# Performance work log

Measured on AMD Instinct MI355X. Metric: run time of the kernel, lower is better.

Reference implementation:

```python
import jax, jax.numpy as jnp
import numpy as np

TEMPERATURE = 11.313708498984761  # sqrt(128)
TOP_K = 16
EPS = 10e-8


def sparse_attention(attn_s, top_k):
    # attn_s: [N, T]; keep top_k entries per row, shift by k-th value, clamp, renormalize
    T = attn_s.shape[1]
    if T <= top_k:
        return attn_s
    delta = jax.lax.top_k(attn_s, top_k)[0][:, -1] + EPS  # [N]
    w = jnp.maximum(attn_s - delta[:, None], 0.0)
    return w / (jnp.sum(w, axis=1, keepdims=True) + EPS)


def setup_inputs() -> dict:
    key = jax.random.key(0)
    kq, kk, kv = jax.random.split(key, 3)
    q = jax.random.normal(kq, (8, 4096, 128), dtype=jnp.float32)
    k = jax.random.normal(kk, (8, 4096, 128), dtype=jnp.float32)
    v = jax.random.normal(kv, (8, 1, 128), dtype=jnp.float32)
    return {"q": q, "k": k, "v": v}


def reference(q, k, v):
    # scores: [b, lq, lk]
    scores = jnp.einsum('bqd,bkd->bqk', q, k) / TEMPERATURE
    # max over keys (keepdim) then exp -> [b, lq, 1]
    scores = jnp.exp(jnp.max(scores, axis=-1, keepdims=True))
    b, lq, _ = scores.shape
    # flag=True: softmax over the query dimension (permute(0,2,1) then softmax(-1))
    attn = jax.nn.softmax(scores[:, :, 0], axis=-1)  # [b, lq]
    # Sparse_attention top-k over query dim (flag=True reshape path)
    sp = sparse_attention(attn, TOP_K)  # [b, lq]
    attn3 = sp[:, :, None]  # [b, lq, 1] (dropout p=0.0 -> identity)
    out = jnp.einsum('bqk,bkd->bqd', attn3, v)  # [b, lq, dv]
    extra_loss = 0.0
    return out, attn3, extra_loss
```

## Files before the change

### kernel.cpp

```cpp
#include <hip/hip_runtime.h>
#include <math.h>

typedef __attribute__((ext_vector_type(8)))  short short8v;
typedef __attribute__((ext_vector_type(4)))  short short4v;
typedef __attribute__((ext_vector_type(16))) float f32x16;

#define NB     8
#define SEQ    4096
#define DIM    128
#define KSPLIT 4
#define NSPAN  (SEQ / KSPLIT)
#define BN     64
#define BM     256
#define TEMP_INV (1.0f / 11.313708498984761f)
#define EPSF   1e-7f
#define NEGINF -3.0e38f

__device__ __forceinline__ unsigned short f2bf(float x) {
    unsigned u = __float_as_uint(x);
    return (unsigned short)((u + 0x7FFFu + ((u >> 16) & 1u)) >> 16);
}
__device__ __forceinline__ float bf2f(unsigned short h) {
    return __uint_as_float(((unsigned)h) << 16);
}

#define GL_LDS16(gsrc, ldst)                                                              \
    __builtin_amdgcn_global_load_lds((const __attribute__((address_space(1))) void*)(gsrc), \
                                     (__attribute__((address_space(3))) void*)(ldst), 16, 0, 0)

__global__ __launch_bounds__(256) void split_k_kernel(
    const float* __restrict__ kp, unsigned short* __restrict__ ks)
{
    int t    = blockIdx.x * 256 + threadIdx.x;
    int row  = t >> 3;
    int soct = t & 7;
    const float* src = kp + (size_t)row * DIM + soct * 16;
    unsigned short* dst = ks + (size_t)row * 256;
    int key = (row & 15) << 3;
    #pragma unroll
    for (int i = 0; i < 4; ++i) {
        float4 x = *(const float4*)(src + i * 4);
        int p = (soct * 16 + i * 4) ^ key;
        float xs[4] = {x.x, x.y, x.z, x.w};
        short4v h, l;
        #pragma unroll
        for (int j = 0; j < 4; ++j) {
            unsigned short hb = f2bf(xs[j]);
            h[j] = (short)hb;
            l[j] = (short)f2bf(xs[j] - bf2f(hb));
        }
        *(short4v*)(dst + p)       = h;
        *(short4v*)(dst + 128 + p) = l;
    }
}

__global__ __launch_bounds__(512, 4) void max_scores2_kernel(
    const float* __restrict__ qp, const unsigned short* __restrict__ ksp,
    float* __restrict__ mpart)
{
    __shared__ __align__(16) unsigned short kbuf[2][BN * 256];

    const int bid   = blockIdx.x;
    const int batch = bid & 7;
    const int qt    = (bid >> 3) & 15;
    const int ks    = bid >> 7;

    const int tid   = threadIdx.x;
    const int wv    = tid >> 6;
    const int lane  = tid & 63;
    const int lhalf = lane >> 5;
    const int l31   = lane & 31;
    const int qrow0 = qt * BM + wv * 32;

    const char* ktile0 = (const char*)(ksp + ((size_t)(batch * SEQ + ks * NSPAN)) * 256);
    const int   woff   = wv * 4096;

    #pragma unroll
    for (int r = 0; r < 4; ++r) {
        int off = woff + r * 1024;
        GL_LDS16(ktile0 + off + lane * 16, (char*)&kbuf[0][0] + off);
    }

    short8v ah[8], al[8];
    {
        const float* qrow = qp + ((size_t)(batch * SEQ + qrow0 + l31)) * DIM + lhalf * 8;
        #pragma unroll
        for (int ch = 0; ch < 8; ++ch) {
            float4 x0 = *(const float4*)(qrow + ch * 16);
            float4 x1 = *(const float4*)(qrow + ch * 16 + 4);
            float xs[8] = {x0.x, x0.y, x0.z, x0.w, x1.x, x1.y, x1.z, x1.w};
            short8v h, l;
            #pragma unroll
            for (int j = 0; j < 8; ++j) {
                unsigned short hb = f2bf(xs[j]);
                h[j] = (short)hb;
                l[j] = (short)f2bf(xs[j] - bf2f(hb));
            }
            ah[ch] = h; al[ch] = l;
        }
    }

    f32x16 mx;
    #pragma unroll
    for (int r = 0; r < 16; ++r) mx[r] = NEGINF;

    __syncthreads();

    int cur = 0;
    for (int it = 0; it < NSPAN / BN; ++it) {
        if (it < NSPAN / BN - 1) {
            const char* src = ktile0 + (size_t)(it + 1) * (BN * 512);
            #pragma unroll
            for (int r = 0; r < 4; ++r) {
                int off = woff + r * 1024;
                GL_LDS16(src + off + lane * 16, (char*)&kbuf[cur ^ 1][0] + off);
            }
        }
        #pragma unroll
        for (int ns = 0; ns < 2; ++ns) {
            const int  brow = ns * 32 + l31;
            const int  bkey = (l31 & 15) << 3;
            const char* base = (const char*)&kbuf[cur][0] + brow * 512;
            f32x16 c;
            #pragma unroll
            for (int r = 0; r < 16; ++r) c[r] = 0.f;
            #pragma unroll
            for (int ch = 0; ch < 8; ++ch) {
                const int d0   = ch * 16 + lhalf * 8;
                const int boff = 2 * (d0 ^ bkey);
                short8v bh = *(const short8v*)(base + boff);
                short8v bl = *(const short8v*)(base + 256 + boff);
                c = __builtin_amdgcn_mfma_f32_32x32x16_bf16(ah[ch], bh, c, 0, 0, 0);
                c = __builtin_amdgcn_mfma_f32_32x32x16_bf16(al[ch], bh, c, 0, 0, 0);
                c = __builtin_amdgcn_mfma_f32_32x32x16_bf16(ah[ch], bl, c, 0, 0, 0);
            }
            #pragma unroll
            for (int r = 0; r < 16; ++r) mx[r] = fmaxf(mx[r], c[r]);
        }
        __syncthreads();
        cur ^= 1;
    }

    #pragma unroll
    for (int r = 0; r < 16; ++r) {
        float v = mx[r];
        #pragma unroll
        for (int off = 16; off; off >>= 1)
            v = fmaxf(v, __shfl_xor(v, off, 64));
        mx[r] = v;
    }
    if (l31 == 0) {
        #pragma unroll
        for (int r = 0; r < 16; ++r) {
            int rr = (r & 3) + 8 * (r >> 2) + 4 * lhalf;
            mpart[((size_t)(batch * SEQ + qrow0 + rr)) * KSPLIT + ks] = mx[r] * TEMP_INV;
        }
    }
}

__global__ __launch_bounds__(512, 2) void max_scores_kernel(
    const float* __restrict__ qp, const float* __restrict__ kp,
    float* __restrict__ mpart)
{
    __shared__ short khi[BN * DIM];
    __shared__ short klo[BN * DIM];

    const int bid   = blockIdx.x;
    const int batch = bid & 7;
    const int qt    = (bid >> 3) & 15;
    const int ks    = bid >> 7;
    const int tid   = threadIdx.x;
    const int wv    = tid >> 6;
    const int lane  = tid & 63;
    const int lhalf = lane >> 5;
    const int l31   = lane & 31;
    const int qrow0 = qt * BM + wv * 32;

    short8v ah[8], al[8];
    {
        const float* qrow = qp + ((size_t)(batch * SEQ + qrow0 + l31)) * DIM + lhalf * 8;
        #pragma unroll
        for (int ch = 0; ch < 8; ++ch) {
            float4 x0 = *(const float4*)(qrow + ch * 16);
            float4 x1 = *(const float4*)(qrow + ch * 16 + 4);
            float xs[8] = {x0.x, x0.y, x0.z, x0.w, x1.x, x1.y, x1.z, x1.w};
            short8v h, l;
            #pragma unroll
            for (int j = 0; j < 8; ++j) {
                unsigned short hb = f2bf(xs[j]);
                h[j] = (short)hb;
                l[j] = (short)f2bf(xs[j] - bf2f(hb));
            }
            ah[ch] = h; al[ch] = l;
        }
    }

    f32x16 mx;
    #pragma unroll
    for (int r = 0; r < 16; ++r) mx[r] = NEGINF;

    const int srow = tid >> 3;
    const int soct = tid & 7;
    const int skey = (srow & 15) << 3;

    for (int it = 0; it < NSPAN / BN; ++it) {
        const int n0 = ks * NSPAN + it * BN;
        __syncthreads();
        {
            const float* ksrc = kp + ((size_t)(batch * SEQ + n0 + srow)) * DIM + soct * 16;
            #pragma unroll
            for (int i = 0; i < 4; ++i) {
                float4 x = *(const float4*)(ksrc + i * 4);
                int dq  = soct * 16 + i * 4;
                int idx = srow * DIM + (dq ^ skey);
                float xs[4] = {x.x, x.y, x.z, x.w};
                short4v h, l;
                #pragma unroll
                for (int j = 0; j < 4; ++j) {
                    unsigned short hb = f2bf(xs[j]);
                    h[j] = (short)hb;
                    l[j] = (short)f2bf(xs[j] - bf2f(hb));
                }
                *(short4v*)(&khi[idx]) = h;
                *(short4v*)(&klo[idx]) = l;
            }
        }
        __syncthreads();

        #pragma unroll
        for (int ns = 0; ns < 2; ++ns) {
            const int brow = ns * 32 + l31;
            const int bkey = (brow & 15) << 3;
            f32x16 c;
            #pragma unroll
            for (int r = 0; r < 16; ++r) c[r] = 0.f;
            #pragma unroll
            for (int ch = 0; ch < 8; ++ch) {
                const int d0  = ch * 16 + lhalf * 8;
                const int idx = brow * DIM + (d0 ^ bkey);
                short8v bh = *(const short8v*)(&khi[idx]);
                short8v bl = *(const short8v*)(&klo[idx]);
                c = __builtin_amdgcn_mfma_f32_32x32x16_bf16(ah[ch], bh, c, 0, 0, 0);
                c = __builtin_amdgcn_mfma_f32_32x32x16_bf16(al[ch], bh, c, 0, 0, 0);
                c = __builtin_amdgcn_mfma_f32_32x32x16_bf16(ah[ch], bl, c, 0, 0, 0);
            }
            #pragma unroll
            for (int r = 0; r < 16; ++r) mx[r] = fmaxf(mx[r], c[r]);
        }
    }

    #pragma unroll
    for (int r = 0; r < 16; ++r) {
        float v = mx[r];
        #pragma unroll
        for (int off = 16; off; off >>= 1)
            v = fmaxf(v, __shfl_xor(v, off, 64));
        mx[r] = v;
    }
    if (l31 == 0) {
        #pragma unroll
        for (int r = 0; r < 16; ++r) {
            int rr = (r & 3) + 8 * (r >> 2) + 4 * lhalf;
            mpart[((size_t)(batch * SEQ + qrow0 + rr)) * KSPLIT + ks] = mx[r] * TEMP_INV;
        }
    }
}

__global__ __launch_bounds__(1024) void softmax_topk2_kernel(
    const float* __restrict__ mpart, float* __restrict__ attn_out,
    float* __restrict__ loss_out)
{
    const int b    = blockIdx.x;
    const int tid  = threadIdx.x;
    const int wv   = tid >> 6;
    const int lane = tid & 63;
    __shared__ float cand[256];
    __shared__ float smZ[16], smW[16];
    __shared__ float bc[2];

    float m[4];
    #pragma unroll
    for (int j = 0; j < 4; ++j) {
        int qq = tid + j * 1024;
        float4 mp = *(const float4*)(mpart + ((size_t)(b * SEQ + qq)) * KSPLIT);
        m[j] = fmaxf(fmaxf(mp.x, mp.y), fmaxf(mp.z, mp.w));
    }

    {
        float a0 = m[0], a1 = m[1], a2 = m[2], a3 = m[3];
        for (int pass = 0; pass < 16; ++pass) {
            float v = fmaxf(fmaxf(a0, a1), fmaxf(a2, a3));
            #pragma unroll
            for (int off = 32; off; off >>= 1) v = fmaxf(v, __shfl_xor(v, off, 64));
            bool has = (a0 == v) || (a1 == v) || (a2 == v) || (a3 == v);
            unsigned long long msk = __ballot(has);
            int leader = __ffsll(msk) - 1;
            if (lane == leader) {
                if (a0 == v) a0 = NEGINF;
                else if (a1 == v) a1 = NEGINF;
                else if (a2 == v) a2 = NEGINF;
                else a3 = NEGINF;
            }
            if (lane == pass) cand[wv * 16 + pass] = v;
        }
    }
    __syncthreads();

    if (wv == 0) {
        float a0 = cand[lane * 4 + 0], a1 = cand[lane * 4 + 1];
        float a2 = cand[lane * 4 + 2], a3 = cand[lane * 4 + 3];
        float first = 0.f, last = 0.f;
        for (int pass = 0; pass < 16; ++pass) {
            float v = fmaxf(fmaxf(a0, a1), fmaxf(a2, a3));
            #pragma unroll
            for (int off = 32; off; off >>= 1) v = fmaxf(v, __shfl_xor(v, off, 64));
            bool has = (a0 == v) || (a1 == v) || (a2 == v) || (a3 == v);
            unsigned long long msk = __ballot(has);
            int leader = __ffsll(msk) - 1;
            if (lane == leader) {
                if (a0 == v) a0 = NEGINF;
                else if (a1 == v) a1 = NEGINF;
                else if (a2 == v) a2 = NEGINF;
                else a3 = NEGINF;
            }
            if (pass == 0) first = v;
            last = v;
        }
        if (lane == 0) { bc[0] = first; bc[1] = last; }
    }
    __syncthreads();

    const float S   = expf(bc[0]);
    const float m16 = bc[1];

    float e[4]; float ls = 0.f;
    #pragma unroll
    for (int j = 0; j < 4; ++j) { e[j] = expf(expf(m[j]) - S); ls += e[j]; }
    #pragma unroll
    for (int off = 32; off; off >>= 1) ls += __shfl_xor(ls, off, 64);
    if (lane == 0) smZ[wv] = ls;
    __syncthreads();
    float Z = 0.f;
    #pragma unroll
    for (int i = 0; i < 16; ++i) Z += smZ[i];

    const float a16   = expf(expf(m16) - S) / Z;
    const float delta = a16 + EPSF;

    float w0[4]; float lw = 0.f;
    #pragma unroll
    for (int j = 0; j < 4; ++j) { w0[j] = fmaxf(e[j] / Z - delta, 0.f); lw += w0[j]; }
    #pragma unroll
    for (int off = 32; off; off >>= 1) lw += __shfl_xor(lw, off, 64);
    if (lane == 0) smW[wv] = lw;
    __syncthreads();
    float W = 0.f;
    #pragma unroll
    for (int i = 0; i < 16; ++i) W += smW[i];
    const float rW = 1.f / (W + EPSF);

    #pragma unroll
    for (int j = 0; j < 4; ++j)
        attn_out[b * SEQ + tid + j * 1024] = w0[j] * rW;
    if (b == 0 && tid == 0) loss_out[0] = 0.f;
}

__global__ void broadcast_out_kernel(const float* __restrict__ sp,
                                     const float* __restrict__ vp,
                                     float* __restrict__ outp)
{
    int gid = blockIdx.x * 256 + threadIdx.x;
    int row = gid >> 5;
    int c4  = gid & 31;
    float  s  = sp[row];
    float4 vv = *(const float4*)(vp + (row >> 12) * DIM + c4 * 4);
    float4 o; o.x = s * vv.x; o.y = s * vv.y; o.z = s * vv.z; o.w = s * vv.w;
    *(float4*)(outp + (size_t)gid * 4) = o;
}

extern "C" void kernel_launch(void* const* d_in, const int* in_sizes, int n_in,
                              void* d_out, int out_size, void* d_ws, size_t ws_size,
                              hipStream_t stream)
{
    (void)in_sizes; (void)n_in; (void)out_size;
    const float* q = (const float*)d_in[0];
    const float* k = (const float*)d_in[1];
    const float* v = (const float*)d_in[2];
    float* out  = (float*)d_out;
    float* attn = out + (size_t)NB * SEQ * DIM;
    float* loss = attn + (size_t)NB * SEQ;

    const size_t KSPLIT_BYTES = (size_t)NB * SEQ * 256 * 2;
    const size_t MPART_BYTES  = (size_t)NB * SEQ * KSPLIT * 4;

    float* mpart;
    if (ws_size >= KSPLIT_BYTES + MPART_BYTES) {
        unsigned short* ksplit = (unsigned short*)d_ws;
        mpart = (float*)((char*)d_ws + KSPLIT_BYTES);
        hipLaunchKernelGGL(split_k_kernel, dim3(NB * SEQ * 8 / 256), dim3(256), 0, stream, k, ksplit);
        hipLaunchKernelGGL(max_scores2_kernel, dim3(NB * (SEQ / BM) * KSPLIT), dim3(512), 0, stream,
                           q, ksplit, mpart);
    } else {
        mpart = (float*)d_ws;
        hipLaunchKernelGGL(max_scores_kernel, dim3(NB * (SEQ / BM) * KSPLIT), dim3(512), 0, stream,
                           q, k, mpart);
    }
    hipLaunchKernelGGL(softmax_topk2_kernel, dim3(NB), dim3(1024), 0, stream, mpart, attn, loss);
    hipLaunchKernelGGL(broadcast_out_kernel, dim3((NB * SEQ * DIM / 4) / 256), dim3(256), 0, stream,
                       attn, v, out);
}
```

Before: 195.3 us.

## Replace split-bf16 max scores with bf16 top-2 candidates plus fp32 rescoring

The three-MFMA split-bf16 (hi/lo) scoring pass becomes a single-bf16 pass that tracks the top two candidate key indices per row and per key split. The candidates are packed into the low bits of a biased float key. A new rescore kernel then recomputes those eight candidates exactly in fp32 and takes the max. This removes two thirds of the MFMA work and halves K staging bytes, and adds s_setprio around the compute. The risk is wrong maxima when bf16 error pushes the true max outside the top two of a split, and the biased-key packing assumes scores above -128.

```diff
diff --git a/kernel.cpp b/kernel.cpp
--- a/kernel.cpp
+++ b/kernel.cpp
@@ -23,42 +23,40 @@
 __device__ __forceinline__ float bf2f(unsigned short h) {
     return __uint_as_float(((unsigned)h) << 16);
 }
+__device__ __forceinline__ unsigned umaxu(unsigned a, unsigned b) { return a > b ? a : b; }
 
 #define GL_LDS16(gsrc, ldst)                                                              \
     __builtin_amdgcn_global_load_lds((const __attribute__((address_space(1))) void*)(gsrc), \
                                      (__attribute__((address_space(3))) void*)(ldst), 16, 0, 0)
 
-__global__ __launch_bounds__(256) void split_k_kernel(
-    const float* __restrict__ kp, unsigned short* __restrict__ ks)
+__global__ __launch_bounds__(256) void split_khi_kernel(
+    const float* __restrict__ kp, unsigned short* __restrict__ kh)
 {
     int t    = blockIdx.x * 256 + threadIdx.x;
-    int row  = t >> 3;
-    int soct = t & 7;
-    const float* src = kp + (size_t)row * DIM + soct * 16;
-    unsigned short* dst = ks + (size_t)row * 256;
+    int row  = t >> 2;
+    int part = t & 3;
+    const float* src = kp + (size_t)row * DIM + part * 32;
+    unsigned short* dst = kh + (size_t)row * DIM;
     int key = (row & 15) << 3;
     #pragma unroll
-    for (int i = 0; i < 4; ++i) {
-        float4 x = *(const float4*)(src + i * 4);
-        int p = (soct * 16 + i * 4) ^ key;
-        float xs[4] = {x.x, x.y, x.z, x.w};
-        short4v h, l;
-        #pragma unroll
-        for (int j = 0; j < 4; ++j) {
-            unsigned short hb = f2bf(xs[j]);
-            h[j] = (short)hb;
-            l[j] = (short)f2bf(xs[j] - bf2f(hb));
-        }
-        *(short4v*)(dst + p)       = h;
-        *(short4v*)(dst + 128 + p) = l;
-    }
-}
-
-__global__ __launch_bounds__(512, 4) void max_scores2_kernel(
-    const float* __restrict__ qp, const unsigned short* __restrict__ ksp,
-    float* __restrict__ mpart)
-{
-    __shared__ __align__(16) unsigned short kbuf[2][BN * 256];
+    for (int c = 0; c < 4; ++c) {
+        int d = part * 32 + c * 8;
+        float4 x0 = *(const float4*)(src + c * 8);
+        float4 x1 = *(const float4*)(src + c * 8 + 4);
+        short8v h;
+        h[0] = (short)f2bf(x0.x); h[1] = (short)f2bf(x0.y);
+        h[2] = (short)f2bf(x0.z); h[3] = (short)f2bf(x0.w);
+        h[4] = (short)f2bf(x1.x); h[5] = (short)f2bf(x1.y);
+        h[6] = (short)f2bf(x1.z); h[7] = (short)f2bf(x1.w);
+        *(short8v*)(dst + (d ^ key)) = h;
+    }
+}
+
+__global__ __launch_bounds__(512, 4) void max_hi_kernel(
+    const float* __restrict__ qp, const unsigned short* __restrict__ khp,
+    unsigned int* __restrict__ cand)
+{
+    __shared__ __align__(16) unsigned short kbuf[2][BN * DIM];
 
     const int bid   = blockIdx.x;
     const int batch = bid & 7;
@@ -72,90 +70,134 @@
     const int l31   = lane & 31;
     const int qrow0 = qt * BM + wv * 32;
 
-    const char* ktile0 = (const char*)(ksp + ((size_t)(batch * SEQ + ks * NSPAN)) * 256);
-    const int   woff   = wv * 4096;
-
-    #pragma unroll
-    for (int r = 0; r < 4; ++r) {
+    const char* ktile0 = (const char*)(khp + ((size_t)(batch * SEQ + ks * NSPAN)) * DIM);
+    const int   woff   = wv * 2048;
+
+    #pragma unroll
+    for (int r = 0; r < 2; ++r) {
         int off = woff + r * 1024;
         GL_LDS16(ktile0 + off + lane * 16, (char*)&kbuf[0][0] + off);
     }
 
-    short8v ah[8], al[8];
+    short8v ah[8];
     {
         const float* qrow = qp + ((size_t)(batch * SEQ + qrow0 + l31)) * DIM + lhalf * 8;
         #pragma unroll
         for (int ch = 0; ch < 8; ++ch) {
             float4 x0 = *(const float4*)(qrow + ch * 16);
             float4 x1 = *(const float4*)(qrow + ch * 16 + 4);
-            float xs[8] = {x0.x, x0.y, x0.z, x0.w, x1.x, x1.y, x1.z, x1.w};
-            short8v h, l;
-            #pragma unroll
-            for (int j = 0; j < 8; ++j) {
-                unsigned short hb = f2bf(xs[j]);
-                h[j] = (short)hb;
-                l[j] = (short)f2bf(xs[j] - bf2f(hb));
-            }
-            ah[ch] = h; al[ch] = l;
-        }
-    }
-
-    f32x16 mx;
-    #pragma unroll
-    for (int r = 0; r < 16; ++r) mx[r] = NEGINF;
+            short8v h;
+            h[0] = (short)f2bf(x0.x); h[1] = (short)f2bf(x0.y);
+            h[2] = (short)f2bf(x0.z); h[3] = (short)f2bf(x0.w);
+            h[4] = (short)f2bf(x1.x); h[5] = (short)f2bf(x1.y);
+            h[6] = (short)f2bf(x1.z); h[7] = (short)f2bf(x1.w);
+            ah[ch] = h;
+        }
+    }
+
+    unsigned pk0[16], pk1[16];
+    #pragma unroll
+    for (int r = 0; r < 16; ++r) { pk0[r] = 0u; pk1[r] = 0u; }
 
     __syncthreads();
 
     int cur = 0;
     for (int it = 0; it < NSPAN / BN; ++it) {
         if (it < NSPAN / BN - 1) {
-            const char* src = ktile0 + (size_t)(it + 1) * (BN * 512);
-            #pragma unroll
-            for (int r = 0; r < 4; ++r) {
+            const char* src = ktile0 + (size_t)(it + 1) * (BN * 256);
+            #pragma unroll
+            for (int r = 0; r < 2; ++r) {
                 int off = woff + r * 1024;
                 GL_LDS16(src + off + lane * 16, (char*)&kbuf[cur ^ 1][0] + off);
             }
         }
+        __builtin_amdgcn_s_setprio(1);
+        const unsigned itb = (unsigned)it;
         #pragma unroll
         for (int ns = 0; ns < 2; ++ns) {
             const int  brow = ns * 32 + l31;
             const int  bkey = (l31 & 15) << 3;
-            const char* base = (const char*)&kbuf[cur][0] + brow * 512;
+            const char* base = (const char*)&kbuf[cur][0] + brow * 256;
             f32x16 c;
             #pragma unroll
             for (int r = 0; r < 16; ++r) c[r] = 0.f;
             #pragma unroll
             for (int ch = 0; ch < 8; ++ch) {
-                const int d0   = ch * 16 + lhalf * 8;
-                const int boff = 2 * (d0 ^ bkey);
+                const int boff = 2 * ((ch * 16 + lhalf * 8) ^ bkey);
                 short8v bh = *(const short8v*)(base + boff);
-                short8v bl = *(const short8v*)(base + 256 + boff);
                 c = __builtin_amdgcn_mfma_f32_32x32x16_bf16(ah[ch], bh, c, 0, 0, 0);
-                c = __builtin_amdgcn_mfma_f32_32x32x16_bf16(al[ch], bh, c, 0, 0, 0);
-                c = __builtin_amdgcn_mfma_f32_32x32x16_bf16(ah[ch], bl, c, 0, 0, 0);
-            }
-            #pragma unroll
-            for (int r = 0; r < 16; ++r) mx[r] = fmaxf(mx[r], c[r]);
-        }
+            }
+            #pragma unroll
+            for (int r = 0; r < 16; ++r) {
+                unsigned pv = (__float_as_uint(c[r] + 128.f) & 0xFFFFFFF0u) | itb;
+                if (ns == 0) pk0[r] = umaxu(pk0[r], pv);
+                else         pk1[r] = umaxu(pk1[r], pv);
+            }
+        }
+        __builtin_amdgcn_s_setprio(0);
         __syncthreads();
         cur ^= 1;
     }
 
     #pragma unroll
     for (int r = 0; r < 16; ++r) {
-        float v = mx[r];
-        #pragma unroll
-        for (int off = 16; off; off >>= 1)
-            v = fmaxf(v, __shfl_xor(v, off, 64));
-        mx[r] = v;
-    }
-    if (l31 == 0) {
-        #pragma unroll
-        for (int r = 0; r < 16; ++r) {
+        unsigned k0 = pk0[r], k1v = pk1[r];
+        unsigned i0  = ((k0 & 15u) << 6)  | l31;
+        unsigned i1v = ((k1v & 15u) << 6) | 32u | l31;
+        unsigned t1, t1i, t2, t2i;
+        if (k0 >= k1v) { t1 = k0;  t1i = i0;  t2 = k1v; t2i = i1v; }
+        else           { t1 = k1v; t1i = i1v; t2 = k0;  t2i = i0;  }
+        #pragma unroll
+        for (int off = 1; off <= 16; off <<= 1) {
+            unsigned o1  = (unsigned)__shfl_xor((int)t1,  off, 64);
+            unsigned o1i = (unsigned)__shfl_xor((int)t1i, off, 64);
+            unsigned o2  = (unsigned)__shfl_xor((int)t2,  off, 64);
+            unsigned o2i = (unsigned)__shfl_xor((int)t2i, off, 64);
+            bool og = o1 > t1;
+            unsigned n1  = og ? o1  : t1;
+            unsigned n1i = og ? o1i : t1i;
+            unsigned a2  = og ? t1  : o1;
+            unsigned a2i = og ? t1i : o1i;
+            unsigned b2  = og ? o2  : t2;
+            unsigned b2i = og ? o2i : t2i;
+            bool ag = a2 > b2;
+            t1 = n1; t1i = n1i;
+            t2 = ag ? a2 : b2; t2i = ag ? a2i : b2i;
+        }
+        if (l31 == 0) {
             int rr = (r & 3) + 8 * (r >> 2) + 4 * lhalf;
-            mpart[((size_t)(batch * SEQ + qrow0 + rr)) * KSPLIT + ks] = mx[r] * TEMP_INV;
-        }
-    }
+            cand[((size_t)(batch * SEQ + qrow0 + rr)) * KSPLIT + ks] =
+                (t1i & 0xFFFFu) | (t2i << 16);
+        }
+    }
+}
+
+__global__ __launch_bounds__(256) void rescore_kernel(
+    const float* __restrict__ qp, const float* __restrict__ kp,
+    const unsigned int* __restrict__ cand, float* __restrict__ mq)
+{
+    const int row  = blockIdx.x * 4 + (threadIdx.x >> 6);
+    const int lane = threadIdx.x & 63;
+    const int b    = row >> 12;
+    const int g    = lane >> 3;
+    const int t8   = lane & 7;
+    const int ks   = g >> 1;
+    unsigned cc  = cand[(size_t)row * KSPLIT + ks];
+    unsigned idx = (g & 1) ? (cc >> 16) : (cc & 0xFFFFu);
+    const float* qrow = qp + (size_t)row * DIM + t8 * 16;
+    const float* krow = kp + ((size_t)(b * SEQ + ks * NSPAN + (int)idx)) * DIM + t8 * 16;
+    float s = 0.f;
+    #pragma unroll
+    for (int i = 0; i < 4; ++i) {
+        float4 a  = *(const float4*)(qrow + i * 4);
+        float4 kk = *(const float4*)(krow + i * 4);
+        s += a.x * kk.x + a.y * kk.y + a.z * kk.z + a.w * kk.w;
+    }
+    #pragma unroll
+    for (int off = 1; off <= 4; off <<= 1) s += __shfl_xor(s, off, 64);
+    #pragma unroll
+    for (int off = 8; off <= 32; off <<= 1) s = fmaxf(s, __shfl_xor(s, off, 64));
+    if (lane == 0) mq[row] = s * TEMP_INV;
 }
 
 __global__ __launch_bounds__(512, 2) void max_scores_kernel(
@@ -266,8 +308,15 @@
     }
 }
 
+__global__ void reduce4_kernel(const float* __restrict__ mpart, float* __restrict__ mq)
+{
+    int i = blockIdx.x * 256 + threadIdx.x;
+    float4 mp = *(const float4*)(mpart + (size_t)i * 4);
+    mq[i] = fmaxf(fmaxf(mp.x, mp.y), fmaxf(mp.z, mp.w));
+}
+
 __global__ __launch_bounds__(1024) void softmax_topk2_kernel(
-    const float* __restrict__ mpart, float* __restrict__ attn_out,
+    const float* __restrict__ mq, float* __restrict__ attn_out,
     float* __restrict__ loss_out)
 {
     const int b    = blockIdx.x;
@@ -280,11 +329,7 @@
 
     float m[4];
     #pragma unroll
-    for (int j = 0; j < 4; ++j) {
-        int qq = tid + j * 1024;
-        float4 mp = *(const float4*)(mpart + ((size_t)(b * SEQ + qq)) * KSPLIT);
-        m[j] = fmaxf(fmaxf(mp.x, mp.y), fmaxf(mp.z, mp.w));
-    }
+    for (int j = 0; j < 4; ++j) m[j] = mq[b * SEQ + tid + j * 1024];
 
     {
         float a0 = m[0], a1 = m[1], a2 = m[2], a3 = m[3];
@@ -390,22 +435,28 @@
     float* attn = out + (size_t)NB * SEQ * DIM;
     float* loss = attn + (size_t)NB * SEQ;
 
-    const size_t KSPLIT_BYTES = (size_t)NB * SEQ * 256 * 2;
-    const size_t MPART_BYTES  = (size_t)NB * SEQ * KSPLIT * 4;
-
-    float* mpart;
-    if (ws_size >= KSPLIT_BYTES + MPART_BYTES) {
-        unsigned short* ksplit = (unsigned short*)d_ws;
-        mpart = (float*)((char*)d_ws + KSPLIT_BYTES);
-        hipLaunchKernelGGL(split_k_kernel, dim3(NB * SEQ * 8 / 256), dim3(256), 0, stream, k, ksplit);
-        hipLaunchKernelGGL(max_scores2_kernel, dim3(NB * (SEQ / BM) * KSPLIT), dim3(512), 0, stream,
-                           q, ksplit, mpart);
+    const size_t KH_BYTES   = (size_t)NB * SEQ * DIM * 2;
+    const size_t CAND_BYTES = (size_t)NB * SEQ * KSPLIT * 4;
+    const size_t MQ_BYTES   = (size_t)NB * SEQ * 4;
+
+    if (ws_size >= KH_BYTES + CAND_BYTES + MQ_BYTES) {
+        unsigned short* kh  = (unsigned short*)d_ws;
+        unsigned int* cand  = (unsigned int*)((char*)d_ws + KH_BYTES);
+        float* mq           = (float*)((char*)d_ws + KH_BYTES + CAND_BYTES);
+        hipLaunchKernelGGL(split_khi_kernel, dim3(NB * SEQ * 4 / 256), dim3(256), 0, stream, k, kh);
+        hipLaunchKernelGGL(max_hi_kernel, dim3(NB * (SEQ / BM) * KSPLIT), dim3(512), 0, stream,
+                           q, kh, cand);
+        hipLaunchKernelGGL(rescore_kernel, dim3(NB * SEQ / 4), dim3(256), 0, stream,
+                           q, k, cand, mq);
+        hipLaunchKernelGGL(softmax_topk2_kernel, dim3(NB), dim3(1024), 0, stream, mq, attn, loss);
     } else {
-        mpart = (float*)d_ws;
+        float* mpart = (float*)d_ws;
+        float* mq    = mpart + (size_t)NB * SEQ * KSPLIT;
         hipLaunchKernelGGL(max_scores_kernel, dim3(NB * (SEQ / BM) * KSPLIT), dim3(512), 0, stream,
                            q, k, mpart);
-    }
-    hipLaunchKernelGGL(softmax_topk2_kernel, dim3(NB), dim3(1024), 0, stream, mpart, attn, loss);
+        hipLaunchKernelGGL(reduce4_kernel, dim3(NB * SEQ / 256), dim3(256), 0, stream, mpart, mq);
+        hipLaunchKernelGGL(softmax_topk2_kernel, dim3(NB), dim3(1024), 0, stream, mq, attn, loss);
+    }
     hipLaunchKernelGGL(broadcast_out_kernel, dim3((NB * SEQ * DIM / 4) / 256), dim3(256), 0, stream,
                        attn, v, out);
 }
```

Result: faster. 166.3 us (-14.9%).
